# Performance work log

Hardware: AMD Instinct MI355X
Metric: run time of the kernel (lower is better)

Reference implementation:

```python
import math
import jax, jax.numpy as jnp
import numpy as np

B, N, F, K = 4, 4096, 128, 32
EPS = 1e-8  # tsl.epsilon
TEMP0, TEMP_DECAY = 1.0, 0.99995


def setup_inputs() -> dict:
    key = jax.random.key(0)
    k1, k2, k3, k4 = jax.random.split(key, 4)
    emb = jax.random.normal(k1, (B, N, F), dtype=jnp.float32)
    adj = jax.random.uniform(k2, (B, N, N), dtype=jnp.float32)
    logits_param = jax.random.normal(k3, (N, K), dtype=jnp.float32)
    u = jax.random.uniform(k4, (B, N, K), dtype=jnp.float32, minval=1e-9, maxval=1.0)
    gumbel_noise = -jnp.log(-jnp.log(u))
    return {"emb": emb, "adj": adj, "logits_param": logits_param, "gumbel_noise": gumbel_noise}


def reference(emb, adj, logits_param, gumbel_noise):
    # temp decays on each get_temp() call in training mode (called twice per forward)
    t1 = max(TEMP0 * TEMP_DECAY, 0.05)
    t2 = max(t1 * TEMP_DECAY, 0.05)

    # ---- gumbel-softmax hard sample with straight-through estimator ----
    y_soft = jax.nn.softmax(logits_param[None] / t1 + gumbel_noise, axis=-1)  # [B,N,K]
    y_hard = jax.nn.one_hot(jnp.argmax(y_soft, axis=-1), K, dtype=y_soft.dtype)
    s_sample = jax.lax.stop_gradient(y_hard - y_soft) + y_soft + EPS  # [B,N,K]

    # ---- soft assignment for regularizers (unbatched [N,K]) ----
    s_soft = jax.nn.softmax(logits_param / t2, axis=-1)  # [N,K]

    # mincut_num = trace(s^T A s) per batch, without forming [K,K]
    As = jnp.einsum('bnm,mk->bnk', adj, s_soft)            # [B,N,K]
    mincut_num = jnp.einsum('nk,bnk->b', s_soft, As)       # [B]
    # mincut_den = trace(s^T D s): D is diag(deg) -> O(N*K) instead of diag_embed
    d_flat = adj.sum(axis=-1)                              # [B,N]
    mincut_den = jnp.einsum('bn,nk,nk->b', d_flat, s_soft, s_soft)
    mincut_loss = -jnp.mean(mincut_num / mincut_den)

    ss = s_soft.T @ s_soft                                 # [K,K]
    ortho_loss = jnp.linalg.norm(ss / jnp.linalg.norm(ss) - jnp.eye(K, dtype=ss.dtype) / math.sqrt(K))

    # ---- pooling ----
    out_emb = jnp.einsum('bnk,bnf->bkf', s_sample, emb)    # [B,K,F]
    As2 = jnp.einsum('bnm,bml->bnl', adj, s_sample)        # [B,N,K]
    out_adj = jnp.einsum('bnk,bnl->bkl', s_sample, As2)    # [B,K,K]

    out_adj = out_adj * (1.0 - jnp.eye(K, dtype=out_adj.dtype))  # zero diagonal
    d = jnp.sqrt(out_adj.sum(axis=-1, keepdims=True)) + EPS
    out_adj = out_adj / d / jnp.swapaxes(d, -1, -2)

    return out_emb, out_adj, s_sample, mincut_loss, ortho_loss
```

## Files before the change

kernel.cpp:

```cpp
#include <hip/hip_runtime.h>
#include <hip/hip_bf16.h>
#include <math.h>

#define B_ 4
#define N_ 4096
#define F_ 128
#define K_ 32
#define EPS_ 1e-8f

typedef __attribute__((ext_vector_type(8))) __bf16 bf16x8;
typedef __attribute__((ext_vector_type(4))) float f32x4;

#define WS_SSOFT   0
#define WS_SQ      131072
#define WS_SS      135168
#define WS_WF      136192
#define WS_OADJP   660480
#define WS_NUMDEN  1709056
#define WS_PEMB    1711104
#define WS_OADJ    2235392
#define WS_H       2239488

__global__ void k_ssoft(const float* __restrict__ logits, float* __restrict__ s_soft,
                        float* __restrict__ sq, float* __restrict__ ss, float t2) {
  __shared__ float sl[64][33];
  int t = threadIdx.x;
  int rowbase = blockIdx.x * 64;
  if (t < 64) {
    int n = rowbase + t;
    float z[32];
    float mx = -1e30f;
    for (int k = 0; k < 32; ++k) { z[k] = logits[n*32+k] / t2; mx = fmaxf(mx, z[k]); }
    float s = 0.f;
    for (int k = 0; k < 32; ++k) { z[k] = expf(z[k]-mx); s += z[k]; }
    float sqa = 0.f;
    for (int k = 0; k < 32; ++k) {
      float v = z[k] / s;
      s_soft[n*32+k] = v;
      sl[t][k] = v;
      sqa += v*v;
    }
    sq[n] = sqa;
  }
  __syncthreads();
  for (int pp = 0; pp < 4; ++pp) {
    int p = pp*256 + t;
    int k = p >> 5, l = p & 31;
    float a = 0.f;
    for (int r = 0; r < 64; ++r) a += sl[r][k]*sl[r][l];
    atomicAdd(&ss[p], a);
  }
}

__global__ void k_gumbel(const float* __restrict__ logits, const float* __restrict__ gum,
                         float* __restrict__ s_sample, int* __restrict__ h, float t1) {
  int i = blockIdx.x*256 + threadIdx.x;
  int n = i & (N_-1);
  float z[32];
  float mx = -1e30f;
  for (int k = 0; k < 32; ++k) { z[k] = logits[n*32+k]/t1 + gum[(size_t)i*32+k]; mx = fmaxf(mx, z[k]); }
  float s = 0.f;
  for (int k = 0; k < 32; ++k) { z[k] = expf(z[k]-mx); s += z[k]; }
  int am = 0; float best = -1.f;
  for (int k = 0; k < 32; ++k) { z[k] = z[k]/s; if (z[k] > best) { best = z[k]; am = k; } }
  for (int k = 0; k < 32; ++k) {
    float yh = (k==am) ? 1.f : 0.f;
    s_sample[(size_t)i*32+k] = (yh - z[k]) + z[k] + EPS_;
  }
  h[i] = am;
}

__global__ void k_wfrag(const float* __restrict__ s_soft, const int* __restrict__ h,
                        bf16x8* __restrict__ wf) {
  int i = blockIdx.x*256 + threadIdx.x;
  int lane = i & 63;
  int c = (i >> 6) & 3;
  int tt = (i >> 8) & 127;
  int b = i >> 15;
  int col = c*16 + (lane & 15);
  int m0 = tt*32 + (lane >> 4)*8;
  bf16x8 v;
  if (col < 32) {
    for (int j = 0; j < 8; ++j) v[j] = (__bf16)s_soft[(m0+j)*32 + col];
  } else {
    int cc = col - 32;
    for (int j = 0; j < 8; ++j) v[j] = (__bf16)((h[b*N_ + m0 + j] == cc) ? 1.f : 0.f);
  }
  wf[i] = v;
}

#define CVT8(dst, va, vb) { dst[0]=(__bf16)va[0]; dst[1]=(__bf16)va[1]; dst[2]=(__bf16)va[2]; dst[3]=(__bf16)va[3]; \
                            dst[4]=(__bf16)vb[0]; dst[5]=(__bf16)vb[1]; dst[6]=(__bf16)vb[2]; dst[7]=(__bf16)vb[3]; }

#define MFMA8(A0,A1,A2,A3,W0,W1,W2,W3) { \
  bf16x8 af0, af1; CVT8(af0, A0, A1); CVT8(af1, A2, A3); \
  acc00 = __builtin_amdgcn_mfma_f32_16x16x32_bf16(af0, W0, acc00, 0, 0, 0); \
  acc01 = __builtin_amdgcn_mfma_f32_16x16x32_bf16(af0, W1, acc01, 0, 0, 0); \
  acc02 = __builtin_amdgcn_mfma_f32_16x16x32_bf16(af0, W2, acc02, 0, 0, 0); \
  acc03 = __builtin_amdgcn_mfma_f32_16x16x32_bf16(af0, W3, acc03, 0, 0, 0); \
  acc10 = __builtin_amdgcn_mfma_f32_16x16x32_bf16(af1, W0, acc10, 0, 0, 0); \
  acc11 = __builtin_amdgcn_mfma_f32_16x16x32_bf16(af1, W1, acc11, 0, 0, 0); \
  acc12 = __builtin_amdgcn_mfma_f32_16x16x32_bf16(af1, W2, acc12, 0, 0, 0); \
  acc13 = __builtin_amdgcn_mfma_f32_16x16x32_bf16(af1, W3, acc13, 0, 0, 0); }

#define NT(p) __builtin_nontemporal_load((const f32x4*)(p))

__launch_bounds__(256, 4)
__global__ void k_gemm(const float* __restrict__ adj, const bf16x8* __restrict__ wf,
                       const float* __restrict__ s_soft, const float* __restrict__ sq,
                       const int* __restrict__ h, float* __restrict__ numden_p,
                       float* __restrict__ oadjp) {
  __shared__ float oal[1024];
  __shared__ float rn[4], rd[4];
  int t = threadIdx.x;
  int w = t >> 6, l = t & 63;
  int lr = l & 15, lhi = l >> 4;
  int bid = blockIdx.x;
  int sp = bid & 7, r = (bid >> 3) & 31, b = bid >> 8;

  for (int i = t; i < 1024; i += 256) oal[i] = 0.f;
  __syncthreads();

  int row0 = r*128 + w*32;
  int m0 = sp*512;
  const float* pa0 = adj + (size_t)b*N_*N_ + (size_t)(row0 + lr)*N_ + m0 + lhi*8;
  const float* pa1 = pa0 + (size_t)16*N_;
  const bf16x8* pw = wf + ((size_t)b*128 + (m0 >> 5))*256 + l;

  f32x4 acc00 = {0,0,0,0}, acc01 = {0,0,0,0}, acc02 = {0,0,0,0}, acc03 = {0,0,0,0};
  f32x4 acc10 = {0,0,0,0}, acc11 = {0,0,0,0}, acc12 = {0,0,0,0}, acc13 = {0,0,0,0};

  f32x4 xa0 = NT(pa0), xa1 = NT(pa0+4), xa2 = NT(pa1), xa3 = NT(pa1+4);
  f32x4 ya0, ya1, ya2, ya3;
  bf16x8 w0, w1, w2, w3;

  #pragma unroll 1
  for (int it = 0; it < 16; it += 2) {
    ya0 = NT(pa0+32); ya1 = NT(pa0+36); ya2 = NT(pa1+32); ya3 = NT(pa1+36);
    w0 = pw[0]; w1 = pw[64]; w2 = pw[128]; w3 = pw[192];
    MFMA8(xa0, xa1, xa2, xa3, w0, w1, w2, w3);
    pw += 256;
    if (it + 2 < 16) { xa0 = NT(pa0+64); xa1 = NT(pa0+68); xa2 = NT(pa1+64); xa3 = NT(pa1+68); }
    w0 = pw[0]; w1 = pw[64]; w2 = pw[128]; w3 = pw[192];
    MFMA8(ya0, ya1, ya2, ya3, w0, w1, w2, w3);
    pw += 256;
    pa0 += 64; pa1 += 64;
  }

  float numacc = 0.f, denacc = 0.f;
  {
    f32x4 a0s[2] = {acc00, acc10}, a1s[2] = {acc01, acc11};
    f32x4 a2s[2] = {acc02, acc12}, a3s[2] = {acc03, acc13};
    for (int rt = 0; rt < 2; ++rt) {
      int rbase = row0 + rt*16 + lhi*4;
      for (int i = 0; i < 4; ++i) {
        int row = rbase + i;
        float sqv = sq[row];
        int hv = h[b*N_ + row];
        numacc += a0s[rt][i] * s_soft[row*32 + lr];
        numacc += a1s[rt][i] * s_soft[row*32 + 16 + lr];
        float v2 = a2s[rt][i], v3 = a3s[rt][i];
        denacc += (v2 + v3) * sqv;
        atomicAdd(&oal[hv*32 + lr], v2);
        atomicAdd(&oal[hv*32 + 16 + lr], v3);
      }
    }
  }
  for (int off = 32; off; off >>= 1) {
    numacc += __shfl_down(numacc, off);
    denacc += __shfl_down(denacc, off);
  }
  if (l == 0) { rn[w] = numacc; rd[w] = denacc; }
  __syncthreads();
  if (t == 0) {
    numden_p[bid] = rn[0]+rn[1]+rn[2]+rn[3];
    numden_p[1024 + bid] = rd[0]+rd[1]+rd[2]+rd[3];
  }
  for (int i = t; i < 1024; i += 256) oadjp[(size_t)bid*1024 + i] = oal[i];
}

__global__ void k_outemb(const float* __restrict__ emb, const int* __restrict__ h,
                         float* __restrict__ pemb) {
  __shared__ float accl[32*128];
  int t = threadIdx.x;
  for (int i = t; i < 4096; i += 256) accl[i] = 0.f;
  __syncthreads();
  int b = blockIdx.x >> 5;
  int n0 = (blockIdx.x & 31) * 128;
  int f = t & 127, rr = t >> 7;
  for (int it = 0; it < 64; ++it) {
    int n = n0 + it*2 + rr;
    float v = emb[((size_t)b*N_ + n)*F_ + f];
    int hv = h[b*N_ + n];
    atomicAdd(&accl[hv*128 + f], v);
  }
  __syncthreads();
  for (int i = t; i < 4096; i += 256) pemb[(size_t)blockIdx.x*4096 + i] = accl[i];
}

__global__ void k_reduce(const float* __restrict__ oadjp, const float* __restrict__ pemb,
                         float* __restrict__ oadj, float* __restrict__ out_emb) {
  int blk = blockIdx.x;
  if (blk < 16) {
    int i = blk*256 + threadIdx.x;
    int b = i >> 10, ii = i & 1023;
    float s = 0.f;
    const float* p = oadjp + (size_t)(b*256)*1024 + ii;
    for (int j = 0; j < 256; ++j) s += p[(size_t)j*1024];
    oadj[i] = s;
  } else {
    int i = (blk-16)*256 + threadIdx.x;
    int b = i >> 12, ii = i & 4095;
    float s = 0.f;
    const float* p = pemb + (size_t)(b*32)*4096 + ii;
    for (int j = 0; j < 32; ++j) s += p[(size_t)j*4096];
    out_emb[i] = s;
  }
}

__global__ void k_final(const float* __restrict__ numden_p, const float* __restrict__ oadj,
                        const float* __restrict__ ss, float* __restrict__ dout) {
  __shared__ float dsh[128];
  __shared__ float red[256];
  __shared__ float nd[8];
  int t = threadIdx.x;
  if (t < 8) {
    int b = t & 3;
    const float* p = numden_p + (t >> 2)*1024 + b*256;
    float s = 0.f;
    for (int j = 0; j < 256; ++j) s += p[j];
    nd[t] = s;
  }
  if (t >= 64 && t < 192) {
    int i = t - 64;
    int b = i >> 5, k = i & 31;
    float s = 0.f;
    for (int l = 0; l < 32; ++l) if (l != k) s += oadj[b*1024 + k*32 + l];
    dsh[i] = sqrtf(s) + EPS_;
  }
  __syncthreads();
  for (int i = t; i < 4096; i += 256) {
    int b = i >> 10, k = (i >> 5) & 31, l = i & 31;
    float v = (k == l) ? 0.f : oadj[i] / (dsh[b*32+k] * dsh[b*32+l]);
    dout[16384 + i] = v;
  }
  float a = 0.f;
  for (int i = t; i < 1024; i += 256) { float v = ss[i]; a += v*v; }
  red[t] = a; __syncthreads();
  for (int s2 = 128; s2; s2 >>= 1) { if (t < s2) red[t] += red[t+s2]; __syncthreads(); }
  float fro = sqrtf(red[0]);
  __syncthreads();
  float c = 0.f;
  float inv = 1.f / fro;
  float dk = (float)(1.0 / sqrt(32.0));
  for (int i = t; i < 1024; i += 256) {
    int k = i >> 5, l = i & 31;
    float v = ss[i]*inv - ((k == l) ? dk : 0.f);
    c += v*v;
  }
  red[t] = c; __syncthreads();
  for (int s2 = 128; s2; s2 >>= 1) { if (t < s2) red[t] += red[t+s2]; __syncthreads(); }
  if (t == 0) {
    dout[544769] = sqrtf(red[0]);
    float s = 0.f;
    for (int b = 0; b < 4; ++b) s += nd[b] / nd[4+b];
    dout[544768] = -s*0.25f;
  }
}

extern "C" void kernel_launch(void* const* d_in, const int* in_sizes, int n_in,
                              void* d_out, int out_size, void* d_ws, size_t ws_size,
                              hipStream_t stream) {
  const float* emb    = (const float*)d_in[0];
  const float* adj    = (const float*)d_in[1];
  const float* logits = (const float*)d_in[2];
  const float* gum    = (const float*)d_in[3];
  float* out = (float*)d_out;
  float* ws  = (float*)d_ws;

  float t1 = 0.99995f;
  float t2 = (float)(0.99995 * 0.99995);

  float* s_soft = ws + WS_SSOFT;
  float* sq     = ws + WS_SQ;
  float* ss     = ws + WS_SS;
  bf16x8* wf    = (bf16x8*)(ws + WS_WF);
  float* oadjp  = ws + WS_OADJP;
  float* ndp    = ws + WS_NUMDEN;
  float* pemb   = ws + WS_PEMB;
  float* oadj   = ws + WS_OADJ;
  int* hbuf     = (int*)(ws + WS_H);

  (void)hipMemsetAsync(ss, 0, 1024 * sizeof(float), stream);

  k_ssoft <<<64, 256, 0, stream>>>(logits, s_soft, sq, ss, t2);
  k_gumbel<<<64, 256, 0, stream>>>(logits, gum, out + 20480, hbuf, t1);
  k_wfrag <<<512, 256, 0, stream>>>(s_soft, hbuf, wf);
  k_gemm  <<<1024, 256, 0, stream>>>(adj, wf, s_soft, sq, hbuf, ndp, oadjp);
  k_outemb<<<128, 256, 0, stream>>>(emb, hbuf, pemb);
  k_reduce<<<80, 256, 0, stream>>>(oadjp, pemb, oadj, out);
  k_final <<<1, 256, 0, stream>>>(ndp, oadj, ss, out);
}
```

Before: 444.8 us.

## Stage adjacency tiles through double-buffered LDS with coalesced row loads

The GEMM kernel now loads the fp32 adjacency tile with each 8 threads covering a contiguous 128-byte row segment. It converts the values to packed bf16 and writes them into a double-buffered, padded LDS tile, from which each wave reads its MFMA A-fragments. Previously each lane read 32-byte strided pieces directly from global memory. The aim is better coalescing of the dominant adj stream, at the cost of LDS traffic and a __syncthreads per k-chunk.

Measured after the change: 441.4 us. Within noise of the previous version (-0.8%).

```diff
diff --git a/kernel.cpp b/kernel.cpp
--- a/kernel.cpp
+++ b/kernel.cpp
@@ -89,27 +89,23 @@
   wf[i] = v;
 }
 
-#define CVT8(dst, va, vb) { dst[0]=(__bf16)va[0]; dst[1]=(__bf16)va[1]; dst[2]=(__bf16)va[2]; dst[3]=(__bf16)va[3]; \
-                            dst[4]=(__bf16)vb[0]; dst[5]=(__bf16)vb[1]; dst[6]=(__bf16)vb[2]; dst[7]=(__bf16)vb[3]; }
-
-#define MFMA8(A0,A1,A2,A3,W0,W1,W2,W3) { \
-  bf16x8 af0, af1; CVT8(af0, A0, A1); CVT8(af1, A2, A3); \
-  acc00 = __builtin_amdgcn_mfma_f32_16x16x32_bf16(af0, W0, acc00, 0, 0, 0); \
-  acc01 = __builtin_amdgcn_mfma_f32_16x16x32_bf16(af0, W1, acc01, 0, 0, 0); \
-  acc02 = __builtin_amdgcn_mfma_f32_16x16x32_bf16(af0, W2, acc02, 0, 0, 0); \
-  acc03 = __builtin_amdgcn_mfma_f32_16x16x32_bf16(af0, W3, acc03, 0, 0, 0); \
-  acc10 = __builtin_amdgcn_mfma_f32_16x16x32_bf16(af1, W0, acc10, 0, 0, 0); \
-  acc11 = __builtin_amdgcn_mfma_f32_16x16x32_bf16(af1, W1, acc11, 0, 0, 0); \
-  acc12 = __builtin_amdgcn_mfma_f32_16x16x32_bf16(af1, W2, acc12, 0, 0, 0); \
-  acc13 = __builtin_amdgcn_mfma_f32_16x16x32_bf16(af1, W3, acc13, 0, 0, 0); }
-
 #define NT(p) __builtin_nontemporal_load((const f32x4*)(p))
+
+union PK2 { __bf16 h[2]; unsigned int u; };
+union FR8 { unsigned int u[4]; bf16x8 v; };
+
+static __device__ __forceinline__ unsigned int pk2(float a, float b) {
+  PK2 x; x.h[0] = (__bf16)a; x.h[1] = (__bf16)b; return x.u;
+}
+
+#define LSTRIDE 17
 
 __launch_bounds__(256, 4)
 __global__ void k_gemm(const float* __restrict__ adj, const bf16x8* __restrict__ wf,
                        const float* __restrict__ s_soft, const float* __restrict__ sq,
                        const int* __restrict__ h, float* __restrict__ numden_p,
                        float* __restrict__ oadjp) {
+  __shared__ unsigned int lds[2][128*LSTRIDE];
   __shared__ float oal[1024];
   __shared__ float rn[4], rd[4];
   int t = threadIdx.x;
@@ -119,40 +115,89 @@
   int sp = bid & 7, r = (bid >> 3) & 31, b = bid >> 8;
 
   for (int i = t; i < 1024; i += 256) oal[i] = 0.f;
-  __syncthreads();
-
-  int row0 = r*128 + w*32;
+
+  int row0 = r*128;
   int m0 = sp*512;
-  const float* pa0 = adj + (size_t)b*N_*N_ + (size_t)(row0 + lr)*N_ + m0 + lhi*8;
-  const float* pa1 = pa0 + (size_t)16*N_;
+
+  int rowL = t >> 3;
+  int colf = (t & 7) * 4;
+  const float* pA = adj + (size_t)b*N_*N_ + (size_t)(row0 + rowL)*N_ + m0 + colf;
   const bf16x8* pw = wf + ((size_t)b*128 + (m0 >> 5))*256 + l;
 
   f32x4 acc00 = {0,0,0,0}, acc01 = {0,0,0,0}, acc02 = {0,0,0,0}, acc03 = {0,0,0,0};
   f32x4 acc10 = {0,0,0,0}, acc11 = {0,0,0,0}, acc12 = {0,0,0,0}, acc13 = {0,0,0,0};
 
-  f32x4 xa0 = NT(pa0), xa1 = NT(pa0+4), xa2 = NT(pa1), xa3 = NT(pa1+4);
-  f32x4 ya0, ya1, ya2, ya3;
-  bf16x8 w0, w1, w2, w3;
+  f32x4 ar0 = NT(pA);
+  f32x4 ar1 = NT(pA + (size_t)32*N_);
+  f32x4 ar2 = NT(pA + (size_t)64*N_);
+  f32x4 ar3 = NT(pA + (size_t)96*N_);
+  bf16x8 wc0 = pw[0], wc1 = pw[64], wc2 = pw[128], wc3 = pw[192];
+
+  {
+    int base = rowL*LSTRIDE + (t & 7)*2;
+    lds[0][base]                 = pk2(ar0[0], ar0[1]);
+    lds[0][base+1]               = pk2(ar0[2], ar0[3]);
+    lds[0][base+32*LSTRIDE]      = pk2(ar1[0], ar1[1]);
+    lds[0][base+32*LSTRIDE+1]    = pk2(ar1[2], ar1[3]);
+    lds[0][base+64*LSTRIDE]      = pk2(ar2[0], ar2[1]);
+    lds[0][base+64*LSTRIDE+1]    = pk2(ar2[2], ar2[3]);
+    lds[0][base+96*LSTRIDE]      = pk2(ar3[0], ar3[1]);
+    lds[0][base+96*LSTRIDE+1]    = pk2(ar3[2], ar3[3]);
+  }
+  __syncthreads();
+
+  bf16x8 wn0, wn1, wn2, wn3;
+  int af0base = (w*32 + lr)*LSTRIDE + lhi*4;
+  int af1base = (w*32 + 16 + lr)*LSTRIDE + lhi*4;
 
   #pragma unroll 1
-  for (int it = 0; it < 16; it += 2) {
-    ya0 = NT(pa0+32); ya1 = NT(pa0+36); ya2 = NT(pa1+32); ya3 = NT(pa1+36);
-    w0 = pw[0]; w1 = pw[64]; w2 = pw[128]; w3 = pw[192];
-    MFMA8(xa0, xa1, xa2, xa3, w0, w1, w2, w3);
-    pw += 256;
-    if (it + 2 < 16) { xa0 = NT(pa0+64); xa1 = NT(pa0+68); xa2 = NT(pa1+64); xa3 = NT(pa1+68); }
-    w0 = pw[0]; w1 = pw[64]; w2 = pw[128]; w3 = pw[192];
-    MFMA8(ya0, ya1, ya2, ya3, w0, w1, w2, w3);
-    pw += 256;
-    pa0 += 64; pa1 += 64;
+  for (int c = 0; c < 16; ++c) {
+    int cur = c & 1;
+    if (c < 15) {
+      pA += 32;
+      ar0 = NT(pA);
+      ar1 = NT(pA + (size_t)32*N_);
+      ar2 = NT(pA + (size_t)64*N_);
+      ar3 = NT(pA + (size_t)96*N_);
+      pw += 256;
+      wn0 = pw[0]; wn1 = pw[64]; wn2 = pw[128]; wn3 = pw[192];
+    }
+    FR8 fa0, fa1;
+    fa0.u[0] = lds[cur][af0base];   fa0.u[1] = lds[cur][af0base+1];
+    fa0.u[2] = lds[cur][af0base+2]; fa0.u[3] = lds[cur][af0base+3];
+    fa1.u[0] = lds[cur][af1base];   fa1.u[1] = lds[cur][af1base+1];
+    fa1.u[2] = lds[cur][af1base+2]; fa1.u[3] = lds[cur][af1base+3];
+    acc00 = __builtin_amdgcn_mfma_f32_16x16x32_bf16(fa0.v, wc0, acc00, 0, 0, 0);
+    acc01 = __builtin_amdgcn_mfma_f32_16x16x32_bf16(fa0.v, wc1, acc01, 0, 0, 0);
+    acc02 = __builtin_amdgcn_mfma_f32_16x16x32_bf16(fa0.v, wc2, acc02, 0, 0, 0);
+    acc03 = __builtin_amdgcn_mfma_f32_16x16x32_bf16(fa0.v, wc3, acc03, 0, 0, 0);
+    acc10 = __builtin_amdgcn_mfma_f32_16x16x32_bf16(fa1.v, wc0, acc10, 0, 0, 0);
+    acc11 = __builtin_amdgcn_mfma_f32_16x16x32_bf16(fa1.v, wc1, acc11, 0, 0, 0);
+    acc12 = __builtin_amdgcn_mfma_f32_16x16x32_bf16(fa1.v, wc2, acc12, 0, 0, 0);
+    acc13 = __builtin_amdgcn_mfma_f32_16x16x32_bf16(fa1.v, wc3, acc13, 0, 0, 0);
+    if (c < 15) {
+      int nxt = cur ^ 1;
+      int base = rowL*LSTRIDE + (t & 7)*2;
+      lds[nxt][base]                 = pk2(ar0[0], ar0[1]);
+      lds[nxt][base+1]               = pk2(ar0[2], ar0[3]);
+      lds[nxt][base+32*LSTRIDE]      = pk2(ar1[0], ar1[1]);
+      lds[nxt][base+32*LSTRIDE+1]    = pk2(ar1[2], ar1[3]);
+      lds[nxt][base+64*LSTRIDE]      = pk2(ar2[0], ar2[1]);
+      lds[nxt][base+64*LSTRIDE+1]    = pk2(ar2[2], ar2[3]);
+      lds[nxt][base+96*LSTRIDE]      = pk2(ar3[0], ar3[1]);
+      lds[nxt][base+96*LSTRIDE+1]    = pk2(ar3[2], ar3[3]);
+      wc0 = wn0; wc1 = wn1; wc2 = wn2; wc3 = wn3;
+    }
+    __syncthreads();
   }
 
   float numacc = 0.f, denacc = 0.f;
   {
     f32x4 a0s[2] = {acc00, acc10}, a1s[2] = {acc01, acc11};
     f32x4 a2s[2] = {acc02, acc12}, a3s[2] = {acc03, acc13};
+    int wrow0 = row0 + w*32;
     for (int rt = 0; rt < 2; ++rt) {
-      int rbase = row0 + rt*16 + lhi*4;
+      int rbase = wrow0 + rt*16 + lhi*4;
       for (int i = 0; i < 4; ++i) {
         int row = rbase + i;
         float sqv = sq[row];
```
